# Kernel tuning notes

Measured on AMD Instinct MI355X. Metric: run time of the kernel, lower is better.

## Reference

```python
import jax, jax.numpy as jnp
import numpy as np

NUM_NODES = 100
WINDOW = 128
GH = 256       # graph_hidden_channels
DH = 64        # discrepancy_hidden_channels
OUT = 128      # out_channels
B = 256        # graphs per batch
N = B * NUM_NODES
E = 409600


def _mconv(x, w, b):
    # x: [B, n, W], w: [n, 2, k], b: [n, 2]  (per-node Conv1d(1,2,k), 'same' padding)
    k = w.shape[-1]
    W = x.shape[-1]
    p = k // 2
    xp = jnp.pad(x, ((0, 0), (0, 0), (p, p)))
    win = jnp.stack([xp[..., j:j + W] for j in range(k)], axis=-1)  # [B,n,W,k]
    return jnp.einsum('bnwk,nck->bncw', win, w) + b[None, :, :, None]


def _gcn(x, edge_index, Wg, bg):
    # PyG GCNConv: add self-loops, symmetric normalization, then linear
    Nn = x.shape[0]
    xw = x @ Wg.T
    loops = jnp.arange(Nn, dtype=edge_index.dtype)
    src = jnp.concatenate([edge_index[0], loops])
    dst = jnp.concatenate([edge_index[1], loops])
    deg = jax.ops.segment_sum(jnp.ones(src.shape[0], dtype=xw.dtype), dst, num_segments=Nn)
    norm = jax.lax.rsqrt(jnp.maximum(deg, 1e-12))
    coef = norm[src] * norm[dst]
    agg = jax.ops.segment_sum(coef[:, None] * xw[src], dst, num_segments=Nn)
    return agg + bg


def setup_inputs() -> dict:
    key = jax.random.key(0)
    ks = jax.random.split(key, 20)
    f = 6 * WINDOW
    s = lambda d: 1.0 / np.sqrt(d)
    inp = {
        'x1': jax.random.normal(ks[0], (N, WINDOW), jnp.float32),
        'x2': jax.random.normal(ks[1], (N, WINDOW), jnp.float32),
        'edge_index1': jax.random.randint(ks[2], (2, E), 0, N, jnp.int32),
        'edge_index2': jax.random.randint(ks[3], (2, E), 0, N, jnp.int32),
        'w3': jax.random.normal(ks[4], (NUM_NODES, 2, 3), jnp.float32) * s(3),
        'b3': jax.random.normal(ks[5], (NUM_NODES, 2), jnp.float32) * s(3),
        'w5': jax.random.normal(ks[6], (NUM_NODES, 2, 5), jnp.float32) * s(5),
        'b5': jax.random.normal(ks[7], (NUM_NODES, 2), jnp.float32) * s(5),
        'w7': jax.random.normal(ks[8], (NUM_NODES, 2, 7), jnp.float32) * s(7),
        'b7': jax.random.normal(ks[9], (NUM_NODES, 2), jnp.float32) * s(7),
        'Wff': jax.random.normal(ks[10], (NUM_NODES, GH, f), jnp.float32) * s(f),
        'bff': jax.random.normal(ks[11], (NUM_NODES, GH), jnp.float32) * s(f),
        'Wg': jax.random.normal(ks[12], (GH, GH), jnp.float32) * s(GH),
        'bg': jax.random.normal(ks[13], (GH,), jnp.float32) * s(GH),
        'Wd': jax.random.normal(ks[14], (NUM_NODES, DH, 2 * GH), jnp.float32) * s(2 * GH),
        'bd': jax.random.normal(ks[15], (NUM_NODES, DH), jnp.float32) * s(2 * GH),
        'Wfc': jax.random.normal(ks[16], (OUT, NUM_NODES * DH), jnp.float32) * s(NUM_NODES * DH),
        'bfc': jax.random.normal(ks[17], (OUT,), jnp.float32) * s(NUM_NODES * DH),
    }
    return inp


def reference(x1, x2, edge_index1, edge_index2, w3, b3, w5, b5, w7, b7,
              Wff, bff, Wg, bg, Wd, bd, Wfc, bfc):
    n = w3.shape[0]
    Nn, W = x1.shape
    Bg = Nn // n

    def branch(x):
        xg = x.reshape(Bg, n, W)
        # multiscale CNN: concat conv3/conv5/conv7 along channel -> [B,n,6,W]
        c = jnp.concatenate([_mconv(xg, w3, b3), _mconv(xg, w5, b5), _mconv(xg, w7, b7)], axis=2)
        c = jax.nn.relu(c.reshape(Bg, n, 6 * W))            # channel-major flatten (matches view(-1))
        h = jax.nn.relu(jnp.einsum('bnf,nhf->bnh', c, Wff) + bff)
        return h.reshape(Nn, -1)

    h1 = jax.nn.relu(_gcn(branch(x1), edge_index1, Wg, bg))
    h2 = jax.nn.relu(_gcn(branch(x2), edge_index2, Wg, bg))
    H = h1.shape[-1]
    cat = jnp.concatenate([h1.reshape(Bg, n, H), h2.reshape(Bg, n, H)], axis=-1)  # [B,n,2H]
    d = jnp.einsum('bnf,ndf->bnd', cat, Wd) + bd            # per-node discrepancy FC
    du = jax.nn.relu(d.reshape(Bg, -1))                     # node-major -> [B, n*DH]
    return du @ Wfc.T + bfc
```

## Files before the change

### kernel.cpp

```cpp
#include <hip/hip_runtime.h>

#define DI __device__ __forceinline__

typedef __bf16 bf16_t;
typedef bf16_t bf16x8 __attribute__((ext_vector_type(8)));
typedef float f32x4 __attribute__((ext_vector_type(4)));
typedef ushort ushort8v __attribute__((ext_vector_type(8)));

static constexpr int NNODE = 100, WIN = 128, GH = 256, DH = 64, OUTC = 128, NB = 256;
static constexpr int NTOT = NB * NNODE;
static constexpr int NE = 409600;
static constexpr int FFK = 6 * WIN;
static constexpr size_t CB = (size_t)NNODE * NB * FFK;
static constexpr size_t HB = (size_t)NTOT * GH;
static constexpr int CVT_BLKS = 4064;
static constexpr int NSEG = 64, SEGE = NE / NSEG;
static constexpr int NPK = NTOT / 2;
static constexpr int NRANGE = 4, RDST = NTOT / NRANGE;
static constexpr int RPK = RDST / 2;
static constexpr int HIST_BLKS = 2 * NSEG * NRANGE;

DI ushort f2bf(float f) {
  union { float f; unsigned u; } v; v.f = f;
  unsigned r = v.u + 0x7fffu + ((v.u >> 16) & 1u);
  return (ushort)(r >> 16);
}
DI float bf2f(ushort s) {
  union { unsigned u; float f; } v; v.u = ((unsigned)s) << 16; return v.f;
}
DI float u2f(uint u) { union { uint u; float f; } v; v.u = u; return v.f; }

DI void gload16(const void* g, void* l) {
  __builtin_amdgcn_global_load_lds((const __attribute__((address_space(1))) void*)g,
                                   (__attribute__((address_space(3))) void*)l, 16, 0, 0);
}


DI void cvt_body(int bx, const float* s0, const float* s1, const float* s2,
                 ushort* d0, ushort* d1, ushort* d2) {
  int j = bx * 256 + threadIdx.x;
  const float* s; ushort* d;
  if (j < 3276800 / 4) { s = s0; d = d0; }
  else if ((j -= 3276800 / 4) < 819200 / 4) { s = s1; d = d1; }
  else { j -= 819200 / 4; s = s2; d = d2; }
  float4 v = reinterpret_cast<const float4*>(s)[j];
  ushort4 o;
  o.x = f2bf(v.x); o.y = f2bf(v.y); o.z = f2bf(v.z); o.w = f2bf(v.w);
  reinterpret_cast<ushort4*>(d)[j] = o;
}

DI void histseg_body(int bx, const int* e1d, const int* e2d,
                     ushort* rank_local, uint* segcnt, uint* cnt ) {
  int set = bx & 1, seg = (bx >> 1) & (NSEG - 1), range = bx >> 7;
  int tid = threadIdx.x;
  for (int k = tid; k < RPK; k += 256) cnt[k] = 0;
  __syncthreads();
  const int* dstp = (set ? e2d : e1d) + seg * SEGE;
  ushort* rl = rank_local + set * NE + seg * SEGE;
  const int dbase = range * RDST;
#pragma unroll
  for (int k = 0; k < SEGE / 256; ++k) {
    int i = k * 256 + tid;
    uint dl = (uint)(dstp[i] - dbase);
    if (dl < (uint)RDST) {
      uint sh = (dl & 1) * 16;
      uint old = atomicAdd(&cnt[dl >> 1], 1u << sh);
      rl[i] = (ushort)((old >> sh) & 0xffffu);
    }
  }
  __syncthreads();
  uint* sc = segcnt + (size_t)(set * NSEG + seg) * NPK + range * RPK;
  for (int k = tid; k < RPK; k += 256) sc[k] = cnt[k];
}

DI void fill_body(int bx, const int* e1, const int* e2, const int* offs,
                  const ushort* rank_local, const uint* segbase, int* csr) {
  int i = bx * 256 + threadIdx.x;
  int set = i >= NE;
  int ii = i - set * NE;
  const int* e = set ? e2 : e1;
  int d = e[NE + ii];
  int seg = ii / SEGE;
  uint b32 = segbase[(size_t)(set * NSEG + seg) * NPK + (d >> 1)];
  int base = (b32 >> ((d & 1) * 16)) & 0xffff;
  int pos = offs[set * (NTOT + 1) + d] + base + rank_local[i];
  csr[set * NE + pos] = e[ii];
}

DI void segscan_body(int set, int pb, const uint* segcnt, uint* segbase, int* deg) {
  int p = pb * 256 + threadIdx.x;
  uint lo = 0, hi = 0;
  const uint* sc = segcnt + (size_t)set * NSEG * NPK + p;
  uint* sb = segbase + (size_t)set * NSEG * NPK + p;
  for (int s = 0; s < NSEG; ++s) {
    uint v = sc[(size_t)s * NPK];
    sb[(size_t)s * NPK] = lo | (hi << 16);
    lo += v & 0xffffu; hi += v >> 16;
  }
  reinterpret_cast<int2*>(deg)[set * NPK + p] = make_int2((int)lo, (int)hi);
}

DI void scan_body(int set, const int* deg_, int* offs_, float* norm_) {
  const int* deg = deg_ + set * NTOT;
  int* offs = offs_ + set * (NTOT + 1);
  float* norm = norm_ + set * NTOT;
  __shared__ int part[256];
  int t = threadIdx.x;
  int base = t * 100;
  int s = 0;
  for (int j = 0; j < 100; ++j) s += deg[base + j];
  part[t] = s;
  __syncthreads();
  for (int d = 1; d < 256; d <<= 1) {
    int vv = (t >= d) ? part[t - d] : 0;
    __syncthreads();
    part[t] += vv;
    __syncthreads();
  }
  int run = (t > 0) ? part[t - 1] : 0;
  for (int j = 0; j < 100; ++j) {
    int dv = deg[base + j];
    offs[base + j] = run;
    norm[base + j] = rsqrtf((float)(dv + 1));
    run += dv;
  }
  if (t == 255) offs[NTOT] = part[255];
}

DI void conv_body(int bx, const float* x1, const float* x2,
                  const float* w3, const float* b3, const float* w5, const float* b5,
                  const float* w7, const float* b7, ushort* c, float* xs ) {
  const int t = threadIdx.x;
  const int rowi = t >> 4;
  const int idx = t & 15;
  int r = bx * 16 + rowi;
  int br = r >= NTOT;
  int rr = r - br * NTOT;
  const float* x = br ? x2 : x1;
  int b = rr / 100, node = rr - b * 100;

  float* row = xs + rowi * 136;
  const int w0 = idx * 8;
  float4 v0 = *reinterpret_cast<const float4*>(x + (size_t)rr * WIN + w0);
  float4 v1 = *reinterpret_cast<const float4*>(x + (size_t)rr * WIN + w0 + 4);
  *reinterpret_cast<float4*>(&row[4 + w0]) = v0;
  *reinterpret_cast<float4*>(&row[4 + w0 + 4]) = v1;
  if (idx == 0) { row[0] = 0.f; row[1] = 0.f; row[2] = 0.f; row[3] = 0.f; }
  if (idx == 15) { row[132] = 0.f; row[133] = 0.f; row[134] = 0.f; row[135] = 0.f; }
  __syncthreads();

  float xv[14];
#pragma unroll
  for (int j = 0; j < 14; ++j) xv[j] = row[1 + w0 + j];

  const float* W3 = w3 + node * 6;  const float* B3 = b3 + node * 2;
  const float* W5 = w5 + node * 10; const float* B5 = b5 + node * 2;
  const float* W7 = w7 + node * 14; const float* B7 = b7 + node * 2;
  ushort* out = c + (size_t)br * CB + (size_t)(node * NB + b) * FFK + w0;

#pragma unroll
  for (int ch = 0; ch < 2; ++ch) {
    float k3[3], k5[5], k7[7];
#pragma unroll
    for (int j = 0; j < 3; ++j) k3[j] = W3[ch * 3 + j];
#pragma unroll
    for (int j = 0; j < 5; ++j) k5[j] = W5[ch * 5 + j];
#pragma unroll
    for (int j = 0; j < 7; ++j) k7[j] = W7[ch * 7 + j];
    float bb3 = B3[ch], bb5 = B5[ch], bb7 = B7[ch];
    ushort8v o3, o5, o7;
#pragma unroll
    for (int p = 0; p < 8; ++p) {
      float a3 = bb3, a5 = bb5, a7 = bb7;
#pragma unroll
      for (int j = 0; j < 3; ++j) a3 += k3[j] * xv[p + 2 + j];
#pragma unroll
      for (int j = 0; j < 5; ++j) a5 += k5[j] * xv[p + 1 + j];
#pragma unroll
      for (int j = 0; j < 7; ++j) a7 += k7[j] * xv[p + j];
      o3[p] = f2bf(fmaxf(a3, 0.f));
      o5[p] = f2bf(fmaxf(a5, 0.f));
      o7[p] = f2bf(fmaxf(a7, 0.f));
    }
    *reinterpret_cast<ushort8v*>(out + (0 + ch) * WIN) = o3;
    *reinterpret_cast<ushort8v*>(out + (2 + ch) * WIN) = o5;
    *reinterpret_cast<ushort8v*>(out + (4 + ch) * WIN) = o7;
  }
}

template <int MODE>
DI void gemm_body(int bx, int by, const ushort* __restrict__ A, const ushort* __restrict__ A2,
                  const ushort* __restrict__ Bm, const float* __restrict__ Bf32,
                  ushort* __restrict__ obf, float* __restrict__ of, const float* __restrict__ bias) {
  constexpr int BN = (MODE == 2) ? 64 : 128;
  constexpr int KT = (MODE == 0) ? 12 : (MODE == 1) ? 4 : (MODE == 2) ? 8 : 4;
  constexpr int LDA = (MODE == 0) ? 768 : (MODE == 1) ? 256 : (MODE == 2) ? 256 : 6400;
  constexpr int LDB = (MODE == 0) ? 768 : (MODE == 1) ? 256 : (MODE == 2) ? 512 : 6400;
  constexpr int MF = (MODE == 2) ? 2 : 4;
  constexpr int NF = 4;

  __shared__ ushort As[128 * 64];
  __shared__ ushort Bs[BN * 64];

  const int tid = threadIdx.x, wv = tid >> 6, lane = tid & 63;
  const int j8 = (((lane & 7) ^ (lane >> 3)) - (lane & 7)) * 8;

  int mt = 0, nt = 0, node = 0, kbase = 0, br = 0;
  if constexpr (MODE == 0) {
    int h = bx;
    int s = (h & 7) * 100 + (h >> 3);
    nt = s & 1; int rest = s >> 1;
    mt = rest & 1; int yy = rest >> 1;
    br = yy >= 100; node = yy - br * 100;
  } else if constexpr (MODE == 1) {
    int h = bx;
    int s = (h & 7) * 100 + (h >> 3);
    nt = s & 1; int rest = s >> 1;
    br = rest >= 200; mt = rest - br * 200;
  } else if constexpr (MODE == 2) { mt = bx; node = by; }
  else { mt = bx; kbase = by * 256; }

  const ushort* Ab = nullptr; const ushort* Bb = nullptr; const float* Bfp = nullptr;
  if constexpr (MODE == 0) { Ab = A + (size_t)br * CB + (size_t)node * (NB * FFK) + (size_t)mt * 128 * FFK;
                             Bfp = Bf32 + (size_t)node * (GH * FFK) + (size_t)nt * 128 * FFK; }
  else if constexpr (MODE == 1) { Ab = A + (size_t)br * HB + (size_t)mt * 128 * GH;
                                  Bb = Bm + (size_t)nt * 128 * GH; }
  else if constexpr (MODE == 2) { Bb = Bm + (size_t)node * (DH * 512); }
  else { Ab = A + (size_t)mt * 128 * 6400 + kbase; Bb = Bm + kbase; }

  const int wr = (MODE == 2) ? wv : (wv >> 1);
  const int wc = (MODE == 2) ? 0 : (wv & 1);

  f32x4 acc[MF][NF] = {};

  for (int kt = 0; kt < KT; ++kt) {
    const int k0 = kt * 64;
    __syncthreads();
#pragma unroll
    for (int it = 0; it < 4; ++it) {
      int rb = it * 32 + wv * 8;
      int row = rb + (lane >> 3);
      const ushort* gp;
      if constexpr (MODE == 2) {
        int b_ = mt * 128 + row;
        const ushort* src = (k0 < 256) ? A : A2;
        gp = src + (size_t)(b_ * NNODE + node) * GH + (k0 & 255) + (lane & 7) * 8 + j8;
      } else {
        gp = Ab + (size_t)row * LDA + k0 + (lane & 7) * 8 + j8;
      }
      gload16(gp, &As[rb * 64]);
    }
    if constexpr (MODE == 0) {
#pragma unroll
      for (int it = 0; it < 4; ++it) {
        int row = it * 32 + (tid >> 3);
        int cc = tid & 7;
        const float* fp = Bfp + (size_t)row * LDB + k0 + cc * 8;
        float4 v0 = *reinterpret_cast<const float4*>(fp);
        float4 v1 = *reinterpret_cast<const float4*>(fp + 4);
        ushort8v o;
        o[0] = f2bf(v0.x); o[1] = f2bf(v0.y); o[2] = f2bf(v0.z); o[3] = f2bf(v0.w);
        o[4] = f2bf(v1.x); o[5] = f2bf(v1.y); o[6] = f2bf(v1.z); o[7] = f2bf(v1.w);
        *reinterpret_cast<ushort8v*>(&Bs[row * 64 + ((cc ^ (row & 7)) * 8)]) = o;
      }
    } else {
#pragma unroll
      for (int it = 0; it < BN / 32; ++it) {
        int rb = it * 32 + wv * 8;
        int row = rb + (lane >> 3);
        gload16(Bb + (size_t)row * LDB + k0 + (lane & 7) * 8 + j8, &Bs[rb * 64]);
      }
    }
    __syncthreads();
#pragma unroll
    for (int kk = 0; kk < 2; ++kk) {
      const int ch8 = ((kk * 4 + (lane >> 4)) ^ (lane & 7)) * 8;
      bf16x8 af[MF], bfr[NF];
#pragma unroll
      for (int m = 0; m < MF; ++m) {
        int rr = wr * (MF * 16) + m * 16 + (lane & 15);
        af[m] = *reinterpret_cast<const bf16x8*>(&As[rr * 64 + ch8]);
      }
#pragma unroll
      for (int n = 0; n < NF; ++n) {
        int rr = wc * 64 + n * 16 + (lane & 15);
        bfr[n] = *reinterpret_cast<const bf16x8*>(&Bs[rr * 64 + ch8]);
      }
#pragma unroll
      for (int m = 0; m < MF; ++m)
#pragma unroll
        for (int n = 0; n < NF; ++n)
          acc[m][n] = __builtin_amdgcn_mfma_f32_16x16x32_bf16(af[m], bfr[n], acc[m][n], 0, 0, 0);
    }
  }

  const int lrow = (lane >> 4) * 4, lcol = lane & 15;
#pragma unroll
  for (int m = 0; m < MF; ++m) {
#pragma unroll
    for (int n = 0; n < NF; ++n) {
      int cc = wc * 64 + n * 16 + lcol;
#pragma unroll
      for (int rg = 0; rg < 4; ++rg) {
        int rr = wr * (MF * 16) + m * 16 + lrow + rg;
        float val = acc[m][n][rg];
        if constexpr (MODE == 0) {
          int b_ = mt * 128 + rr;
          int col = nt * 128 + cc;
          val = fmaxf(val + bias[node * GH + col], 0.f);
          obf[(size_t)br * HB + (size_t)(b_ * NNODE + node) * GH + col] = f2bf(val);
        } else if constexpr (MODE == 1) {
          int R = mt * 128 + rr;
          int col = nt * 128 + cc;
          obf[(size_t)br * HB + (size_t)R * GH + col] = f2bf(val * bias[br * NTOT + R]);
        } else if constexpr (MODE == 2) {
          int b_ = mt * 128 + rr;
          val = fmaxf(val + bias[node * DH + cc], 0.f);
          obf[(size_t)b_ * (NNODE * DH) + node * DH + cc] = f2bf(val);
        } else {
          int R = mt * 128 + rr;
          if (by == 0) val += bias[cc];
          atomicAdd(&of[R * OUTC + cc], val);
        }
      }
    }
  }
}


__global__ __launch_bounds__(256) void fused1_k(
    const float* __restrict__ Wd, const float* __restrict__ Wfc, const float* __restrict__ Wg,
    ushort* __restrict__ Wdb, ushort* __restrict__ Wfcb, ushort* __restrict__ Wgb,
    const int* __restrict__ e1d, const int* __restrict__ e2d,
    ushort* __restrict__ rank_local, uint* __restrict__ segcnt,
    const float* __restrict__ x1, const float* __restrict__ x2,
    const float* __restrict__ w3, const float* __restrict__ b3,
    const float* __restrict__ w5, const float* __restrict__ b5,
    const float* __restrict__ w7, const float* __restrict__ b7,
    ushort* __restrict__ c) {
  __shared__ uint smem[RPK];
  int bx = blockIdx.x;
  if (bx < HIST_BLKS) histseg_body(bx, e1d, e2d, rank_local, segcnt, smem);
  else if (bx < HIST_BLKS + 3200) conv_body(bx - HIST_BLKS, x1, x2, w3, b3, w5, b5, w7, b7, c, (float*)smem);
  else cvt_body(bx - HIST_BLKS - 3200, Wd, Wfc, Wg, Wdb, Wfcb, Wgb);
}

__global__ __launch_bounds__(256) void fused3_k(
    const ushort* __restrict__ cbuf, const float* __restrict__ Wff,
    ushort* __restrict__ h, const float* __restrict__ bff,
    const uint* __restrict__ segcnt, uint* __restrict__ segbase, int* __restrict__ deg) {
  if ((int)blockIdx.x < 800)
    gemm_body<0>(blockIdx.x, 0, cbuf, nullptr, nullptr, Wff, h, nullptr, bff);
  else {
    int b = blockIdx.x - 800;
    segscan_body(b / 50, b % 50, segcnt, segbase, deg);
  }
}

__global__ __launch_bounds__(256) void scan_k(const int* __restrict__ deg,
                                              int* __restrict__ offs, float* __restrict__ nrm) {
  scan_body(blockIdx.x, deg, offs, nrm);
}

__global__ __launch_bounds__(256) void fused4_k(
    const ushort* __restrict__ h, const ushort* __restrict__ Wgb,
    ushort* __restrict__ xw, const float* __restrict__ nrm,
    const int* __restrict__ e1, const int* __restrict__ e2,
    const int* __restrict__ offs, const ushort* __restrict__ rank_local,
    const uint* __restrict__ segbase, int* __restrict__ csr) {
  if ((int)blockIdx.x < 800)
    gemm_body<1>(blockIdx.x, 0, h, nullptr, Wgb, nullptr, xw, nullptr, nrm);
  else
    fill_body(blockIdx.x - 800, e1, e2, offs, rank_local, segbase, csr);
}

template <int MODE>
__global__ __launch_bounds__(256) void gemm_k(const ushort* __restrict__ A, const ushort* __restrict__ A2,
                                              const ushort* __restrict__ Bm, ushort* __restrict__ obf,
                                              float* __restrict__ of, const float* __restrict__ bias) {
  gemm_body<MODE>(blockIdx.x, blockIdx.y, A, A2, Bm, nullptr, obf, of, bias);
}

__global__ __launch_bounds__(256) void agg_k(const ushort* __restrict__ xw_, const int* __restrict__ offs_,
                                             const int* __restrict__ csr_, const float* __restrict__ norm_,
                                             const float* __restrict__ bg, ushort* __restrict__ hg_) {
  int bid = blockIdx.x;
  int c = bid & 7;
  int i = bid >> 3;
  int br = c >> 2, slice = c & 3;
  int g = threadIdx.x >> 3;
  int v = i * 32 + g;
  int l8 = threadIdx.x & 7;
  int col = slice * 64 + l8 * 8;

  const ushort* xw = xw_ + (size_t)br * HB;
  const int* offs = offs_ + br * (NTOT + 1);
  const int* csr = csr_ + br * NE;
  const float* norm = norm_ + br * NTOT;
  ushort* hg = hg_ + (size_t)br * HB;
  const uint* base = reinterpret_cast<const uint*>(xw + col);

  float a[8];
  {
    uint4 q = *reinterpret_cast<const uint4*>(base + (size_t)v * (GH / 2));
    a[0] = u2f(q.x << 16); a[1] = u2f(q.x & 0xffff0000u);
    a[2] = u2f(q.y << 16); a[3] = u2f(q.y & 0xffff0000u);
    a[4] = u2f(q.z << 16); a[5] = u2f(q.z & 0xffff0000u);
    a[6] = u2f(q.w << 16); a[7] = u2f(q.w & 0xffff0000u);
  }
  int e0 = offs[v], e1v = offs[v + 1];
  int j = e0;
  for (; j + 1 < e1v; j += 2) {
    int s0 = csr[j], s1 = csr[j + 1];
    uint4 q0 = *reinterpret_cast<const uint4*>(base + (size_t)s0 * (GH / 2));
    uint4 q1 = *reinterpret_cast<const uint4*>(base + (size_t)s1 * (GH / 2));
    a[0] += u2f(q0.x << 16) + u2f(q1.x << 16);
    a[1] += u2f(q0.x & 0xffff0000u) + u2f(q1.x & 0xffff0000u);
    a[2] += u2f(q0.y << 16) + u2f(q1.y << 16);
    a[3] += u2f(q0.y & 0xffff0000u) + u2f(q1.y & 0xffff0000u);
    a[4] += u2f(q0.z << 16) + u2f(q1.z << 16);
    a[5] += u2f(q0.z & 0xffff0000u) + u2f(q1.z & 0xffff0000u);
    a[6] += u2f(q0.w << 16) + u2f(q1.w << 16);
    a[7] += u2f(q0.w & 0xffff0000u) + u2f(q1.w & 0xffff0000u);
  }
  if (j < e1v) {
    int s0 = csr[j];
    uint4 q0 = *reinterpret_cast<const uint4*>(base + (size_t)s0 * (GH / 2));
    a[0] += u2f(q0.x << 16); a[1] += u2f(q0.x & 0xffff0000u);
    a[2] += u2f(q0.y << 16); a[3] += u2f(q0.y & 0xffff0000u);
    a[4] += u2f(q0.z << 16); a[5] += u2f(q0.z & 0xffff0000u);
    a[6] += u2f(q0.w << 16); a[7] += u2f(q0.w & 0xffff0000u);
  }

  float nv = norm[v];
  float4 bb0 = *reinterpret_cast<const float4*>(bg + col);
  float4 bb1 = *reinterpret_cast<const float4*>(bg + col + 4);
  ushort8v o;
  o[0] = f2bf(fmaxf(nv * a[0] + bb0.x, 0.f));
  o[1] = f2bf(fmaxf(nv * a[1] + bb0.y, 0.f));
  o[2] = f2bf(fmaxf(nv * a[2] + bb0.z, 0.f));
  o[3] = f2bf(fmaxf(nv * a[3] + bb0.w, 0.f));
  o[4] = f2bf(fmaxf(nv * a[4] + bb1.x, 0.f));
  o[5] = f2bf(fmaxf(nv * a[5] + bb1.y, 0.f));
  o[6] = f2bf(fmaxf(nv * a[6] + bb1.z, 0.f));
  o[7] = f2bf(fmaxf(nv * a[7] + bb1.w, 0.f));
  *reinterpret_cast<ushort8v*>(hg + (size_t)v * GH + col) = o;
}

extern "C" void kernel_launch(void* const* d_in, const int* in_sizes, int n_in,
                              void* d_out, int out_size, void* d_ws, size_t ws_size,
                              hipStream_t stream) {
  const float* x1 = (const float*)d_in[0];
  const float* x2 = (const float*)d_in[1];
  const int* e1 = (const int*)d_in[2];
  const int* e2 = (const int*)d_in[3];
  const float* w3 = (const float*)d_in[4];  const float* b3 = (const float*)d_in[5];
  const float* w5 = (const float*)d_in[6];  const float* b5 = (const float*)d_in[7];
  const float* w7 = (const float*)d_in[8];  const float* b7 = (const float*)d_in[9];
  const float* Wff = (const float*)d_in[10]; const float* bff = (const float*)d_in[11];
  const float* Wg = (const float*)d_in[12];  const float* bg = (const float*)d_in[13];
  const float* Wd = (const float*)d_in[14];  const float* bd = (const float*)d_in[15];
  const float* Wfc = (const float*)d_in[16]; const float* bfc = (const float*)d_in[17];
  float* out = (float*)d_out;

  char* ws = (char*)d_ws;
  size_t off = 0;
  auto alloc = [&](size_t bytes) -> char* {
    char* p = ws + off;
    off = (off + bytes + 255) & ~(size_t)255;
    return p;
  };
  ushort* Wdb  = (ushort*)alloc(3276800ull * 2);
  ushort* Wfcb = (ushort*)alloc(819200ull * 2);
  ushort* Wgb  = (ushort*)alloc(65536ull * 2);
  ushort* cbuf = (ushort*)alloc(2 * CB * 2);
  ushort* h    = (ushort*)alloc(2 * HB * 2);
  ushort* xw   = (ushort*)alloc(2 * HB * 2);
  int* deg     = (int*)alloc(2 * NTOT * 4);
  int* offs    = (int*)alloc(2 * (NTOT + 1) * 4);
  ushort* rankl = (ushort*)alloc(2 * NE * 2);
  uint* segcnt  = (uint*)alloc((size_t)2 * NSEG * NPK * 4);
  uint* segbase = (uint*)alloc((size_t)2 * NSEG * NPK * 4);
  int* csr     = (int*)alloc(2 * NE * 4);
  float* nrm   = (float*)alloc(2 * NTOT * 4);
  ushort* du = cbuf;

  hipMemsetAsync(out, 0, (size_t)out_size * 4, stream);

  fused1_k<<<HIST_BLKS + 3200 + CVT_BLKS, 256, 0, stream>>>(
      Wd, Wfc, Wg, Wdb, Wfcb, Wgb,
      e1 + NE, e2 + NE, rankl, segcnt,
      x1, x2, w3, b3, w5, b5, w7, b7, cbuf);
  fused3_k<<<900, 256, 0, stream>>>(cbuf, Wff, h, bff, segcnt, segbase, deg);
  scan_k<<<2, 256, 0, stream>>>(deg, offs, nrm);
  fused4_k<<<4000, 256, 0, stream>>>(h, Wgb, xw, nrm, e1, e2, offs, rankl, segbase, csr);

  agg_k<<<6400, 256, 0, stream>>>(xw, offs, csr, nrm, bg, h);

  gemm_k<2><<<dim3(2, 100), 256, 0, stream>>>(h, h + HB, Wdb, du, nullptr, bd);
  gemm_k<3><<<dim3(2, 25), 256, 0, stream>>>(du, nullptr, Wfcb, nullptr, out, bfc);
}
```

Baseline: 227.6 us.

## Halve Wff GEMM N-tile and register-prefetch next fp32 B tile

The per-node feed-forward GEMM (mode 0) now uses 64-wide N tiles instead of 128, doubling its block count from 800 to 1600 so more blocks run concurrently. It also software-prefetches the next k-step's fp32 Wff slice into registers right after the barrier, so global load latency overlaps the MFMA work of the current step. The cost is that each A tile is loaded twice as often and more registers are held for the prefetch buffer, and the launch grid and block-index decode are updated to match.

```diff
diff --git a/kernel.cpp b/kernel.cpp
--- a/kernel.cpp
+++ b/kernel.cpp
@@ -192,12 +192,13 @@
 DI void gemm_body(int bx, int by, const ushort* __restrict__ A, const ushort* __restrict__ A2,
                   const ushort* __restrict__ Bm, const float* __restrict__ Bf32,
                   ushort* __restrict__ obf, float* __restrict__ of, const float* __restrict__ bias) {
-  constexpr int BN = (MODE == 2) ? 64 : 128;
+  constexpr int BN = (MODE == 1 || MODE == 3) ? 128 : 64;
   constexpr int KT = (MODE == 0) ? 12 : (MODE == 1) ? 4 : (MODE == 2) ? 8 : 4;
   constexpr int LDA = (MODE == 0) ? 768 : (MODE == 1) ? 256 : (MODE == 2) ? 256 : 6400;
   constexpr int LDB = (MODE == 0) ? 768 : (MODE == 1) ? 256 : (MODE == 2) ? 512 : 6400;
   constexpr int MF = (MODE == 2) ? 2 : 4;
-  constexpr int NF = 4;
+  constexpr int NF = (MODE == 0) ? 2 : 4;
+  constexpr int NTW = (MODE == 0) ? 64 : 128;
 
   __shared__ ushort As[128 * 64];
   __shared__ ushort Bs[BN * 64];
@@ -208,8 +209,8 @@
   int mt = 0, nt = 0, node = 0, kbase = 0, br = 0;
   if constexpr (MODE == 0) {
     int h = bx;
-    int s = (h & 7) * 100 + (h >> 3);
-    nt = s & 1; int rest = s >> 1;
+    int s = (h & 7) * 200 + (h >> 3);
+    nt = s & 3; int rest = s >> 2;
     mt = rest & 1; int yy = rest >> 1;
     br = yy >= 100; node = yy - br * 100;
   } else if constexpr (MODE == 1) {
@@ -222,7 +223,7 @@
 
   const ushort* Ab = nullptr; const ushort* Bb = nullptr; const float* Bfp = nullptr;
   if constexpr (MODE == 0) { Ab = A + (size_t)br * CB + (size_t)node * (NB * FFK) + (size_t)mt * 128 * FFK;
-                             Bfp = Bf32 + (size_t)node * (GH * FFK) + (size_t)nt * 128 * FFK; }
+                             Bfp = Bf32 + (size_t)node * (GH * FFK) + (size_t)nt * 64 * FFK; }
   else if constexpr (MODE == 1) { Ab = A + (size_t)br * HB + (size_t)mt * 128 * GH;
                                   Bb = Bm + (size_t)nt * 128 * GH; }
   else if constexpr (MODE == 2) { Bb = Bm + (size_t)node * (DH * 512); }
@@ -232,6 +233,17 @@
   const int wc = (MODE == 2) ? 0 : (wv & 1);
 
   f32x4 acc[MF][NF] = {};
+
+  float4 pb[4];
+  const int prow0 = (tid >> 3), pcc = tid & 7;
+  if constexpr (MODE == 0) {
+#pragma unroll
+    for (int it = 0; it < 2; ++it) {
+      const float* fp = Bfp + (size_t)(it * 32 + prow0) * LDB + 0 + pcc * 8;
+      pb[it * 2]     = *reinterpret_cast<const float4*>(fp);
+      pb[it * 2 + 1] = *reinterpret_cast<const float4*>(fp + 4);
+    }
+  }
 
   for (int kt = 0; kt < KT; ++kt) {
     const int k0 = kt * 64;
@@ -252,16 +264,13 @@
     }
     if constexpr (MODE == 0) {
 #pragma unroll
-      for (int it = 0; it < 4; ++it) {
-        int row = it * 32 + (tid >> 3);
-        int cc = tid & 7;
-        const float* fp = Bfp + (size_t)row * LDB + k0 + cc * 8;
-        float4 v0 = *reinterpret_cast<const float4*>(fp);
-        float4 v1 = *reinterpret_cast<const float4*>(fp + 4);
+      for (int it = 0; it < 2; ++it) {
+        int row = it * 32 + prow0;
+        float4 v0 = pb[it * 2], v1 = pb[it * 2 + 1];
         ushort8v o;
         o[0] = f2bf(v0.x); o[1] = f2bf(v0.y); o[2] = f2bf(v0.z); o[3] = f2bf(v0.w);
         o[4] = f2bf(v1.x); o[5] = f2bf(v1.y); o[6] = f2bf(v1.z); o[7] = f2bf(v1.w);
-        *reinterpret_cast<ushort8v*>(&Bs[row * 64 + ((cc ^ (row & 7)) * 8)]) = o;
+        *reinterpret_cast<ushort8v*>(&Bs[row * 64 + ((pcc ^ (row & 7)) * 8)]) = o;
       }
     } else {
 #pragma unroll
@@ -272,6 +281,17 @@
       }
     }
     __syncthreads();
+    if constexpr (MODE == 0) {
+      if (kt + 1 < KT) {
+        const int kn = (kt + 1) * 64;
+#pragma unroll
+        for (int it = 0; it < 2; ++it) {
+          const float* fp = Bfp + (size_t)(it * 32 + prow0) * LDB + kn + pcc * 8;
+          pb[it * 2]     = *reinterpret_cast<const float4*>(fp);
+          pb[it * 2 + 1] = *reinterpret_cast<const float4*>(fp + 4);
+        }
+      }
+    }
 #pragma unroll
     for (int kk = 0; kk < 2; ++kk) {
       const int ch8 = ((kk * 4 + (lane >> 4)) ^ (lane & 7)) * 8;
@@ -283,7 +303,7 @@
       }
 #pragma unroll
       for (int n = 0; n < NF; ++n) {
-        int rr = wc * 64 + n * 16 + (lane & 15);
+        int rr = wc * (NF * 16) + n * 16 + (lane & 15);
         bfr[n] = *reinterpret_cast<const bf16x8*>(&Bs[rr * 64 + ch8]);
       }
 #pragma unroll
@@ -299,14 +319,14 @@
   for (int m = 0; m < MF; ++m) {
 #pragma unroll
     for (int n = 0; n < NF; ++n) {
-      int cc = wc * 64 + n * 16 + lcol;
+      int cc = wc * (NF * 16) + n * 16 + lcol;
 #pragma unroll
       for (int rg = 0; rg < 4; ++rg) {
         int rr = wr * (MF * 16) + m * 16 + lrow + rg;
         float val = acc[m][n][rg];
         if constexpr (MODE == 0) {
           int b_ = mt * 128 + rr;
-          int col = nt * 128 + cc;
+          int col = nt * NTW + cc;
           val = fmaxf(val + bias[node * GH + col], 0.f);
           obf[(size_t)br * HB + (size_t)(b_ * NNODE + node) * GH + col] = f2bf(val);
         } else if constexpr (MODE == 1) {
@@ -349,10 +369,10 @@
     const ushort* __restrict__ cbuf, const float* __restrict__ Wff,
     ushort* __restrict__ h, const float* __restrict__ bff,
     const uint* __restrict__ segcnt, uint* __restrict__ segbase, int* __restrict__ deg) {
-  if ((int)blockIdx.x < 800)
+  if ((int)blockIdx.x < 1600)
     gemm_body<0>(blockIdx.x, 0, cbuf, nullptr, nullptr, Wff, h, nullptr, bff);
   else {
-    int b = blockIdx.x - 800;
+    int b = blockIdx.x - 1600;
     segscan_body(b / 50, b % 50, segcnt, segbase, deg);
   }
 }
@@ -491,7 +511,7 @@
       Wd, Wfc, Wg, Wdb, Wfcb, Wgb,
       e1 + NE, e2 + NE, rankl, segcnt,
       x1, x2, w3, b3, w5, b5, w7, b7, cbuf);
-  fused3_k<<<900, 256, 0, stream>>>(cbuf, Wff, h, bff, segcnt, segbase, deg);
+  fused3_k<<<1700, 256, 0, stream>>>(cbuf, Wff, h, bff, segcnt, segbase, deg);
   scan_k<<<2, 256, 0, stream>>>(deg, offs, nrm);
   fused4_k<<<4000, 256, 0, stream>>>(h, Wgb, xw, nrm, e1, e2, offs, rankl, segbase, csr);
 
```

Measured after the change: 225.5 us, median of 2. About the same (-0.9%).
